# Optimization experiments

Measured on AMD Instinct MI355X. Metric: run time of the kernel, lower is better.

## Reference

```python
import jax, jax.numpy as jnp
import numpy as np

B, D_IN, D_OUT = 8192, 4096, 4096
IN_DIMS = (64, 64)
OUT_DIMS = (64, 64)
# tt_rank_rate=0.5 over dims [64,64,64,64] -> ranks [1,32,1024,32,1]
RANKS = (1, 32, 1024, 32, 1)


def _kaiming_uniform(key, shape):
    # matches nn.init.kaiming_uniform_(a=sqrt(5)) on a (r_prev, d, r) tensor:
    # fan_in = prod(shape[1:]) = d * r, gain = sqrt(2/(1+5)) = sqrt(1/3)
    fan_in = shape[1] * shape[2]
    bound = np.sqrt(1.0 / 3.0) * np.sqrt(3.0 / fan_in)
    return jax.random.uniform(key, shape, jnp.float32, -bound, bound)


def setup_inputs() -> dict:
    key = jax.random.key(0)
    kx, k0, k1, k2, k3, kb = jax.random.split(key, 6)
    dims = list(IN_DIMS) + list(OUT_DIMS)
    shapes = [(RANKS[i], dims[i], RANKS[i + 1]) for i in range(4)]
    x = jax.random.normal(kx, (B, D_IN), jnp.float32)
    core0 = _kaiming_uniform(k0, shapes[0])  # (1, 64, 32)
    core1 = _kaiming_uniform(k1, shapes[1])  # (32, 64, 1024)
    core2 = _kaiming_uniform(k2, shapes[2])  # (1024, 64, 32)
    core3 = _kaiming_uniform(k3, shapes[3])  # (32, 64, 1)
    bb = 1.0 / np.sqrt(D_IN)
    bias = jax.random.uniform(kb, (D_OUT,), jnp.float32, -bb, bb)
    return {"x": x, "core0": core0, "core1": core1, "core2": core2,
            "core3": core3, "bias": bias}


def reference(x, core0, core1, core2, core3, bias):
    b = x.shape[0]
    s = x.reshape(b, IN_DIMS[0], IN_DIMS[1])          # (B, 64, 64)
    # input core 0: contract first input dim (rank-in = 1 squeezed)
    s = jnp.einsum('bcd,cs->bds', s, core0[0])        # (B, 64, 32)
    # input core 1: contract second input dim and rank
    s = jnp.einsum('bcr,rcs->bs', s, core1)           # (B, 1024)
    # output core 2: expand first output dim
    s = jnp.einsum('br,rAs->bAs', s, core2)           # (B, 64, 32)
    # output core 3: expand second output dim (rank-out = 1 squeezed)
    s = jnp.einsum('bAr,rB->bAB', s, core3[..., 0])   # (B, 64, 64)
    return s.reshape(b, -1) + bias                    # (B, 4096)
```

## Files before the change

kernel.cpp:

```cpp
#include <hip/hip_runtime.h>
#include <hip/hip_bf16.h>


typedef _Float16 h4 __attribute__((ext_vector_type(4)));
typedef _Float16 h8 __attribute__((ext_vector_type(8)));
typedef float f32x4 __attribute__((ext_vector_type(4)));

#define BATCH 8192

__device__ __forceinline__ void gld_lds16(const void* g, void* l) {
  __builtin_amdgcn_global_load_lds(
      (__attribute__((address_space(1))) void*)(g),
      (__attribute__((address_space(3))) void*)(l), 16, 0, 0);
}

__global__ __launch_bounds__(256) void transpose_cast2(
    const float* __restrict__ c1, _Float16* __restrict__ W1t,
    const float* __restrict__ c2, _Float16* __restrict__ W2t) {
  __shared__ float t[64][65];
  const int which = blockIdx.z;
  const float* src = which ? c2 : c1;
  _Float16* dst = which ? W2t : W1t;
  const int K = which ? 1024 : 2048, U = which ? 2048 : 1024;
  const int k0 = (which ? blockIdx.y : blockIdx.x) * 64;
  const int u0 = (which ? blockIdx.x : blockIdx.y) * 64;
  const int tx = threadIdx.x & 63, ty = threadIdx.x >> 6;
  for (int i = ty; i < 64; i += 4) {
    const int k = k0 + i;
    const int sr = which ? k : ((k & 31) * 64 + (k >> 5));
    t[i][tx] = src[(size_t)sr * U + u0 + tx];
  }
  __syncthreads();
  for (int i = ty; i < 64; i += 4) {
    dst[(size_t)(u0 + i) * K + k0 + tx] = (_Float16)t[tx][i];
  }
}

__global__ __launch_bounds__(256) void stage2(const float* __restrict__ x,
                                              const float* __restrict__ c0,
                                              _Float16* __restrict__ s1) {
  __shared__ _Float16 xh[4 * 4096];
  __shared__ float c0l[2048];
  const int b0 = blockIdx.x * 4;
  const int tid = threadIdx.x;

  {
    const float4* xg = (const float4*)(x + (size_t)b0 * 4096);
#pragma unroll
    for (int k = 0; k < 16; ++k) {
      float4 v = xg[tid + 256 * k];
      h4 w = {(_Float16)v.x, (_Float16)v.y, (_Float16)v.z, (_Float16)v.w};
      ((h4*)xh)[tid + 256 * k] = w;
    }
    ((float4*)c0l)[tid] = ((const float4*)c0)[tid];
    ((float4*)c0l)[tid + 256] = ((const float4*)c0)[tid + 256];
  }
  __syncthreads();

  const int row = tid >> 6, t6 = tid & 63;
  const int d0 = (t6 >> 3) * 8;
  const int r0 = (t6 & 7) * 4;
  const _Float16* xrow = xh + row * 4096;

  float acc[8][4];
#pragma unroll
  for (int i = 0; i < 8; ++i)
#pragma unroll
    for (int j = 0; j < 4; ++j) acc[i][j] = 0.0f;

  for (int c = 0; c < 64; ++c) {
    h8 xv = *(const h8*)&xrow[c * 64 + d0];
    f32x4 wv = *(const f32x4*)&c0l[c * 32 + r0];
#pragma unroll
    for (int i = 0; i < 8; ++i) {
      const float xf = (float)xv[i];
#pragma unroll
      for (int j = 0; j < 4; ++j) acc[i][j] += xf * wv[j];
    }
  }

  _Float16* s1row = s1 + (size_t)(b0 + row) * 2048;
#pragma unroll
  for (int i = 0; i < 8; ++i) {
    h4 o = {(_Float16)acc[i][0], (_Float16)acc[i][1], (_Float16)acc[i][2],
            (_Float16)acc[i][3]};
    *(h4*)&s1row[(d0 + i) * 32 + r0] = o;
  }
}

template <int M, int N, int K>
__global__ __launch_bounds__(256, 3) void gemm_tn(
    const _Float16* __restrict__ A, const _Float16* __restrict__ Bt,
    _Float16* __restrict__ C) {
  __shared__ _Float16 lA[128 * 64];
  __shared__ _Float16 lB[128 * 64];
  const int bm = blockIdx.x, bn = blockIdx.y;
  const int tid = threadIdx.x;
  const int w = tid >> 6, lane = tid & 63;
  const int wm = (w >> 1) << 6, wn = (w & 1) << 6;
  const int lr = lane & 15, kh = lane >> 4;

  f32x4 acc[4][4] = {};

  const int sr = (w << 5) + (lane >> 3);
  const int sc = ((lane & 7) ^ (lane >> 3)) << 4;
  const char* gA = (const char*)(A + (size_t)(bm * 128 + sr) * K) + sc;
  const char* gB = (const char*)(Bt + (size_t)(bn * 128 + sr) * K) + sc;
  char* lAw = (char*)lA + w * 4096;
  char* lBw = (char*)lB + w * 4096;

  for (int kt = 0; kt < K / 64; ++kt) {
    __syncthreads();
    const size_t go = (size_t)kt * 128;
#pragma unroll
    for (int i = 0; i < 4; ++i) {
      gld_lds16(gA + go + (size_t)(i * 8) * (K * 2), lAw + i * 1024);
      gld_lds16(gB + go + (size_t)(i * 8) * (K * 2), lBw + i * 1024);
    }
    __syncthreads();
#pragma unroll
    for (int kk = 0; kk < 2; ++kk) {
      h8 af[4], bf[4];
#pragma unroll
      for (int m = 0; m < 4; ++m) {
        const int R = wm + m * 16 + lr;
        af[m] = *(const h8*)((const char*)lA + R * 128 +
                             ((((kk << 2) + kh) ^ (R & 7)) << 4));
      }
#pragma unroll
      for (int n = 0; n < 4; ++n) {
        const int R = wn + n * 16 + lr;
        bf[n] = *(const h8*)((const char*)lB + R * 128 +
                             ((((kk << 2) + kh) ^ (R & 7)) << 4));
      }
#pragma unroll
      for (int m = 0; m < 4; ++m)
#pragma unroll
        for (int n = 0; n < 4; ++n)
          acc[m][n] = __builtin_amdgcn_mfma_f32_16x16x32_f16(af[m], bf[n],
                                                             acc[m][n], 0, 0, 0);
    }
  }

#pragma unroll
  for (int m = 0; m < 4; ++m) {
    const int r0 = bm * 128 + wm + m * 16 + kh * 4;
#pragma unroll
    for (int n = 0; n < 4; ++n) {
      const int c0 = bn * 128 + wn + n * 16 + lr;
#pragma unroll
      for (int q = 0; q < 4; ++q)
        C[(size_t)(r0 + q) * N + c0] = (_Float16)acc[m][n][q];
    }
  }
}

template <int M, int K>
__global__ __launch_bounds__(256, 3) void gemm2_fused(
    const _Float16* __restrict__ A, const _Float16* __restrict__ Bt,
    const float* __restrict__ c3, const float* __restrict__ bias,
    float* __restrict__ out) {
  __shared__ _Float16 lds[128 * 128];
  _Float16* lA = lds;
  _Float16* lB = lds + 128 * 64;
  const int bm = blockIdx.x, bn = blockIdx.y;
  const int tid = threadIdx.x;
  const int w = tid >> 6, lane = tid & 63;
  const int wm = (w >> 1) << 6, wn = (w & 1) << 6;
  const int lr = lane & 15, kh = lane >> 4;

  f32x4 acc[4][4] = {};

  const int sr = (w << 5) + (lane >> 3);
  const int sc = ((lane & 7) ^ (lane >> 3)) << 4;
  const char* gA = (const char*)(A + (size_t)(bm * 128 + sr) * K) + sc;
  const char* gB = (const char*)(Bt + (size_t)(bn * 128 + sr) * K) + sc;
  char* lAw = (char*)lA + w * 4096;
  char* lBw = (char*)lB + w * 4096;

  for (int kt = 0; kt < K / 64; ++kt) {
    __syncthreads();
    const size_t go = (size_t)kt * 128;
#pragma unroll
    for (int i = 0; i < 4; ++i) {
      gld_lds16(gA + go + (size_t)(i * 8) * (K * 2), lAw + i * 1024);
      gld_lds16(gB + go + (size_t)(i * 8) * (K * 2), lBw + i * 1024);
    }
    __syncthreads();
#pragma unroll
    for (int kk = 0; kk < 2; ++kk) {
      h8 af[4], bf[4];
#pragma unroll
      for (int m = 0; m < 4; ++m) {
        const int R = wm + m * 16 + lr;
        af[m] = *(const h8*)((const char*)lA + R * 128 +
                             ((((kk << 2) + kh) ^ (R & 7)) << 4));
      }
#pragma unroll
      for (int n = 0; n < 4; ++n) {
        const int R = wn + n * 16 + lr;
        bf[n] = *(const h8*)((const char*)lB + R * 128 +
                             ((((kk << 2) + kh) ^ (R & 7)) << 4));
      }
#pragma unroll
      for (int m = 0; m < 4; ++m)
#pragma unroll
        for (int n = 0; n < 4; ++n)
          acc[m][n] = __builtin_amdgcn_mfma_f32_16x16x32_f16(af[m], bf[n],
                                                             acc[m][n], 0, 0, 0);
    }
  }

  __syncthreads();

  h8 bfe[4];
  float bb[4][4];
#pragma unroll
  for (int n = 0; n < 4; ++n) {
#pragma unroll
    for (int j = 0; j < 8; ++j)
      bfe[n][j] = (_Float16)c3[(kh * 8 + j) * 64 + n * 16 + lr];
#pragma unroll
    for (int a = 0; a < 4; ++a)
      bb[a][n] = bias[bn * 256 + a * 64 + n * 16 + lr];
  }

#pragma unroll
  for (int m = 0; m < 4; ++m) {
    const int Rb = wm + m * 16 + kh * 4;
#pragma unroll
    for (int n = 0; n < 4; ++n) {
      const int cc = wn + n * 16 + lr;
#pragma unroll
      for (int q = 0; q < 4; ++q) {
        const int R = Rb + q;
        const int byte =
            R * 256 + ((((cc >> 3) ^ (R & 7)) << 4) | ((cc & 7) << 1));
        *(_Float16*)((char*)lds + byte) = (_Float16)acc[m][n][q];
      }
    }
  }
  __syncthreads();

  const int wrow = w << 5;
#pragma unroll
  for (int mi = 0; mi < 2; ++mi) {
    const int row = wrow + mi * 16 + lr;
    const int orow0 = bm * 128 + wrow + mi * 16 + kh * 4;
#pragma unroll
    for (int a = 0; a < 4; ++a) {
      h8 af = *(const h8*)((const char*)lds + row * 256 +
                           ((((a << 2) + kh) ^ (row & 7)) << 4));
#pragma unroll
      for (int n = 0; n < 4; ++n) {
        f32x4 d = {};
        d = __builtin_amdgcn_mfma_f32_16x16x32_f16(af, bfe[n], d, 0, 0, 0);
        const int ocol = bn * 256 + a * 64 + n * 16 + lr;
#pragma unroll
        for (int q = 0; q < 4; ++q)
          out[(size_t)(orow0 + q) * 4096 + ocol] = d[q] + bb[a][n];
      }
    }
  }
}

extern "C" void kernel_launch(void* const* d_in, const int* in_sizes, int n_in,
                              void* d_out, int out_size, void* d_ws,
                              size_t ws_size, hipStream_t stream) {
  (void)in_sizes; (void)n_in; (void)out_size; (void)ws_size;
  const float* x     = (const float*)d_in[0];
  const float* core0 = (const float*)d_in[1];
  const float* core1 = (const float*)d_in[2];
  const float* core2 = (const float*)d_in[3];
  const float* core3 = (const float*)d_in[4];
  const float* bias  = (const float*)d_in[5];
  float* out = (float*)d_out;

  char* ws = (char*)d_ws;
  _Float16* s1h = (_Float16*)ws;
  _Float16* s2h = (_Float16*)(ws + 33554432);
  _Float16* W1t = (_Float16*)(ws + 50331648);
  _Float16* W2t = (_Float16*)(ws + 54525952);

  transpose_cast2<<<dim3(32, 16, 2), 256, 0, stream>>>(core1, W1t, core2, W2t);
  stage2<<<BATCH / 4, 256, 0, stream>>>(x, core0, s1h);
  gemm_tn<BATCH, 1024, 2048><<<dim3(BATCH / 128, 1024 / 128), 256, 0, stream>>>(s1h, W1t, s2h);
  gemm2_fused<BATCH, 1024><<<dim3(BATCH / 128, 2048 / 128), 256, 0, stream>>>(s2h, W2t, core3, bias, out);
}
```

Before: 150.0 us.

## Merge GEMMs into triple-buffered 512-thread kernel with 128x256 tiles

Both GEMM kernels become one templated kernel that uses 8 waves per block and 128x256 output tiles. Global-to-LDS loads are triple-buffered so the next tile's loads overlap the current tile's MFMA work, with one barrier per k-step instead of two. It also adds explicit waitcnt, sched_barrier and setprio hints. The 144KB of LDS per block limits occupancy, and fewer blocks in the N dimension lowers the total block count.

Measured after the change: 155.5 us. 1.04x slower.

```diff
diff --git a/kernel.cpp b/kernel.cpp
--- a/kernel.cpp
+++ b/kernel.cpp
@@ -88,174 +88,140 @@
   }
 }
 
-template <int M, int N, int K>
-__global__ __launch_bounds__(256, 3) void gemm_tn(
+template <int K, int CN, bool FUSED>
+__global__ __launch_bounds__(512, 2) void gemm_pipe(
     const _Float16* __restrict__ A, const _Float16* __restrict__ Bt,
-    _Float16* __restrict__ C) {
-  __shared__ _Float16 lA[128 * 64];
-  __shared__ _Float16 lB[128 * 64];
+    _Float16* __restrict__ C, const float* __restrict__ c3,
+    const float* __restrict__ bias, float* __restrict__ out) {
+  __shared__ __align__(16) char lds[3 * 49152];
+  constexpr int NT = K / 64;
   const int bm = blockIdx.x, bn = blockIdx.y;
   const int tid = threadIdx.x;
   const int w = tid >> 6, lane = tid & 63;
-  const int wm = (w >> 1) << 6, wn = (w & 1) << 6;
   const int lr = lane & 15, kh = lane >> 4;
+  const int wmo = (w >> 2) << 6, wno = (w & 3) << 6;
 
   f32x4 acc[4][4] = {};
 
-  const int sr = (w << 5) + (lane >> 3);
-  const int sc = ((lane & 7) ^ (lane >> 3)) << 4;
+  const int sr = tid >> 3;
+  const int sc = ((tid & 7) ^ (sr & 7)) << 4;
   const char* gA = (const char*)(A + (size_t)(bm * 128 + sr) * K) + sc;
-  const char* gB = (const char*)(Bt + (size_t)(bn * 128 + sr) * K) + sc;
-  char* lAw = (char*)lA + w * 4096;
-  char* lBw = (char*)lB + w * 4096;
-
-  for (int kt = 0; kt < K / 64; ++kt) {
+  const char* gB = (const char*)(Bt + (size_t)(bn * 256 + sr) * K) + sc;
+  const size_t rk = (size_t)K * 128;
+  char* lw = lds + (w << 10);
+
+  auto STAGE = [&](int t) {
+    char* b_ = lw + (t % 3) * 49152;
+    const char* ga = gA + (size_t)t * 128;
+    const char* gb = gB + (size_t)t * 128;
+    gld_lds16(ga, b_);
+    gld_lds16(ga + rk, b_ + 8192);
+    gld_lds16(gb, b_ + 16384);
+    gld_lds16(gb + rk, b_ + 24576);
+    gld_lds16(gb + 2 * rk, b_ + 32768);
+    gld_lds16(gb + 3 * rk, b_ + 40960);
+  };
+
+  auto KSTEP = [&](int t) {
+    const char* bufA = lds + (t % 3) * 49152;
+    const char* bufB = bufA + 16384;
+    h8 af[2][4], bf[2][4];
+#pragma unroll
+    for (int kk = 0; kk < 2; ++kk) {
+#pragma unroll
+      for (int m = 0; m < 4; ++m) {
+        const int R = wmo + m * 16 + lr;
+        af[kk][m] = *(const h8*)(bufA + R * 128 +
+                                 ((((kk << 2) + kh) ^ (R & 7)) << 4));
+      }
+#pragma unroll
+      for (int n = 0; n < 4; ++n) {
+        const int R = wno + n * 16 + lr;
+        bf[kk][n] = *(const h8*)(bufB + R * 128 +
+                                 ((((kk << 2) + kh) ^ (R & 7)) << 4));
+      }
+    }
+    asm volatile("s_waitcnt lgkmcnt(0)" ::: "memory");
+    __builtin_amdgcn_sched_barrier(0);
+    __builtin_amdgcn_s_setprio(1);
+#pragma unroll
+    for (int kk = 0; kk < 2; ++kk)
+#pragma unroll
+      for (int m = 0; m < 4; ++m)
+#pragma unroll
+        for (int n = 0; n < 4; ++n)
+          acc[m][n] = __builtin_amdgcn_mfma_f32_16x16x32_f16(
+              af[kk][m], bf[kk][n], acc[m][n], 0, 0, 0);
+    __builtin_amdgcn_s_setprio(0);
+    __builtin_amdgcn_sched_barrier(0);
+  };
+
+  STAGE(0);
+  STAGE(1);
+  for (int t = 0; t < NT - 1; ++t) {
+    asm volatile("s_waitcnt vmcnt(6)" ::: "memory");
+    __builtin_amdgcn_s_barrier();
+    __builtin_amdgcn_sched_barrier(0);
+    if (t < NT - 2) STAGE(t + 2);
+    KSTEP(t);
+  }
+  asm volatile("s_waitcnt vmcnt(0)" ::: "memory");
+  __builtin_amdgcn_s_barrier();
+  __builtin_amdgcn_sched_barrier(0);
+  KSTEP(NT - 1);
+
+  if constexpr (!FUSED) {
+#pragma unroll
+    for (int m = 0; m < 4; ++m) {
+      const int r0 = bm * 128 + wmo + m * 16 + kh * 4;
+#pragma unroll
+      for (int n = 0; n < 4; ++n) {
+        const int c0 = bn * 256 + wno + n * 16 + lr;
+#pragma unroll
+        for (int q = 0; q < 4; ++q)
+          C[(size_t)(r0 + q) * CN + c0] = (_Float16)acc[m][n][q];
+      }
+    }
+  } else {
+    h8 bfe[4];
+    float bb[8][4];
+#pragma unroll
+    for (int n = 0; n < 4; ++n) {
+#pragma unroll
+      for (int j = 0; j < 8; ++j)
+        bfe[n][j] = (_Float16)c3[(kh * 8 + j) * 64 + n * 16 + lr];
+#pragma unroll
+      for (int a = 0; a < 8; ++a)
+        bb[a][n] = bias[(bn * 8 + a) * 64 + n * 16 + lr];
+    }
     __syncthreads();
-    const size_t go = (size_t)kt * 128;
-#pragma unroll
-    for (int i = 0; i < 4; ++i) {
-      gld_lds16(gA + go + (size_t)(i * 8) * (K * 2), lAw + i * 1024);
-      gld_lds16(gB + go + (size_t)(i * 8) * (K * 2), lBw + i * 1024);
+#pragma unroll
+    for (int m = 0; m < 4; ++m) {
+      const int Rb = wmo + m * 16 + kh * 4;
+#pragma unroll
+      for (int n = 0; n < 4; ++n) {
+        const int cc = wno + n * 16 + lr;
+#pragma unroll
+        for (int q = 0; q < 4; ++q) {
+          const int R = Rb + q;
+          *(_Float16*)(lds + R * 512 +
+                       ((((cc >> 3) ^ (R & 7)) << 4) | ((cc & 7) << 1))) =
+              (_Float16)acc[m][n][q];
+        }
+      }
     }
     __syncthreads();
-#pragma unroll
-    for (int kk = 0; kk < 2; ++kk) {
-      h8 af[4], bf[4];
-#pragma unroll
-      for (int m = 0; m < 4; ++m) {
-        const int R = wm + m * 16 + lr;
-        af[m] = *(const h8*)((const char*)lA + R * 128 +
-                             ((((kk << 2) + kh) ^ (R & 7)) << 4));
-      }
-#pragma unroll
-      for (int n = 0; n < 4; ++n) {
-        const int R = wn + n * 16 + lr;
-        bf[n] = *(const h8*)((const char*)lB + R * 128 +
-                             ((((kk << 2) + kh) ^ (R & 7)) << 4));
-      }
-#pragma unroll
-      for (int m = 0; m < 4; ++m)
-#pragma unroll
-        for (int n = 0; n < 4; ++n)
-          acc[m][n] = __builtin_amdgcn_mfma_f32_16x16x32_f16(af[m], bf[n],
-                                                             acc[m][n], 0, 0, 0);
-    }
-  }
-
-#pragma unroll
-  for (int m = 0; m < 4; ++m) {
-    const int r0 = bm * 128 + wm + m * 16 + kh * 4;
-#pragma unroll
-    for (int n = 0; n < 4; ++n) {
-      const int c0 = bn * 128 + wn + n * 16 + lr;
-#pragma unroll
-      for (int q = 0; q < 4; ++q)
-        C[(size_t)(r0 + q) * N + c0] = (_Float16)acc[m][n][q];
-    }
-  }
-}
-
-template <int M, int K>
-__global__ __launch_bounds__(256, 3) void gemm2_fused(
-    const _Float16* __restrict__ A, const _Float16* __restrict__ Bt,
-    const float* __restrict__ c3, const float* __restrict__ bias,
-    float* __restrict__ out) {
-  __shared__ _Float16 lds[128 * 128];
-  _Float16* lA = lds;
-  _Float16* lB = lds + 128 * 64;
-  const int bm = blockIdx.x, bn = blockIdx.y;
-  const int tid = threadIdx.x;
-  const int w = tid >> 6, lane = tid & 63;
-  const int wm = (w >> 1) << 6, wn = (w & 1) << 6;
-  const int lr = lane & 15, kh = lane >> 4;
-
-  f32x4 acc[4][4] = {};
-
-  const int sr = (w << 5) + (lane >> 3);
-  const int sc = ((lane & 7) ^ (lane >> 3)) << 4;
-  const char* gA = (const char*)(A + (size_t)(bm * 128 + sr) * K) + sc;
-  const char* gB = (const char*)(Bt + (size_t)(bn * 128 + sr) * K) + sc;
-  char* lAw = (char*)lA + w * 4096;
-  char* lBw = (char*)lB + w * 4096;
-
-  for (int kt = 0; kt < K / 64; ++kt) {
-    __syncthreads();
-    const size_t go = (size_t)kt * 128;
-#pragma unroll
-    for (int i = 0; i < 4; ++i) {
-      gld_lds16(gA + go + (size_t)(i * 8) * (K * 2), lAw + i * 1024);
-      gld_lds16(gB + go + (size_t)(i * 8) * (K * 2), lBw + i * 1024);
-    }
-    __syncthreads();
-#pragma unroll
-    for (int kk = 0; kk < 2; ++kk) {
-      h8 af[4], bf[4];
-#pragma unroll
-      for (int m = 0; m < 4; ++m) {
-        const int R = wm + m * 16 + lr;
-        af[m] = *(const h8*)((const char*)lA + R * 128 +
-                             ((((kk << 2) + kh) ^ (R & 7)) << 4));
-      }
-#pragma unroll
-      for (int n = 0; n < 4; ++n) {
-        const int R = wn + n * 16 + lr;
-        bf[n] = *(const h8*)((const char*)lB + R * 128 +
-                             ((((kk << 2) + kh) ^ (R & 7)) << 4));
-      }
-#pragma unroll
-      for (int m = 0; m < 4; ++m)
-#pragma unroll
-        for (int n = 0; n < 4; ++n)
-          acc[m][n] = __builtin_amdgcn_mfma_f32_16x16x32_f16(af[m], bf[n],
-                                                             acc[m][n], 0, 0, 0);
-    }
-  }
-
-  __syncthreads();
-
-  h8 bfe[4];
-  float bb[4][4];
-#pragma unroll
-  for (int n = 0; n < 4; ++n) {
-#pragma unroll
-    for (int j = 0; j < 8; ++j)
-      bfe[n][j] = (_Float16)c3[(kh * 8 + j) * 64 + n * 16 + lr];
-#pragma unroll
-    for (int a = 0; a < 4; ++a)
-      bb[a][n] = bias[bn * 256 + a * 64 + n * 16 + lr];
-  }
-
-#pragma unroll
-  for (int m = 0; m < 4; ++m) {
-    const int Rb = wm + m * 16 + kh * 4;
-#pragma unroll
-    for (int n = 0; n < 4; ++n) {
-      const int cc = wn + n * 16 + lr;
-#pragma unroll
-      for (int q = 0; q < 4; ++q) {
-        const int R = Rb + q;
-        const int byte =
-            R * 256 + ((((cc >> 3) ^ (R & 7)) << 4) | ((cc & 7) << 1));
-        *(_Float16*)((char*)lds + byte) = (_Float16)acc[m][n][q];
-      }
-    }
-  }
-  __syncthreads();
-
-  const int wrow = w << 5;
-#pragma unroll
-  for (int mi = 0; mi < 2; ++mi) {
-    const int row = wrow + mi * 16 + lr;
-    const int orow0 = bm * 128 + wrow + mi * 16 + kh * 4;
-#pragma unroll
-    for (int a = 0; a < 4; ++a) {
-      h8 af = *(const h8*)((const char*)lds + row * 256 +
-                           ((((a << 2) + kh) ^ (row & 7)) << 4));
+    const int row = (w << 4) + lr;
+    const int orow0 = bm * 128 + (w << 4) + (kh << 2);
+#pragma unroll
+    for (int a = 0; a < 8; ++a) {
+      h8 afv = *(const h8*)(lds + row * 512 +
+                            ((((a << 2) + kh) ^ (row & 7)) << 4));
 #pragma unroll
       for (int n = 0; n < 4; ++n) {
         f32x4 d = {};
-        d = __builtin_amdgcn_mfma_f32_16x16x32_f16(af, bfe[n], d, 0, 0, 0);
-        const int ocol = bn * 256 + a * 64 + n * 16 + lr;
+        d = __builtin_amdgcn_mfma_f32_16x16x32_f16(afv, bfe[n], d, 0, 0, 0);
+        const int ocol = (bn * 8 + a) * 64 + n * 16 + lr;
 #pragma unroll
         for (int q = 0; q < 4; ++q)
           out[(size_t)(orow0 + q) * 4096 + ocol] = d[q] + bb[a][n];
@@ -284,6 +250,8 @@
 
   transpose_cast2<<<dim3(32, 16, 2), 256, 0, stream>>>(core1, W1t, core2, W2t);
   stage2<<<BATCH / 4, 256, 0, stream>>>(x, core0, s1h);
-  gemm_tn<BATCH, 1024, 2048><<<dim3(BATCH / 128, 1024 / 128), 256, 0, stream>>>(s1h, W1t, s2h);
-  gemm2_fused<BATCH, 1024><<<dim3(BATCH / 128, 2048 / 128), 256, 0, stream>>>(s2h, W2t, core3, bias, out);
-}
+  gemm_pipe<2048, 1024, false><<<dim3(BATCH / 128, 4), 512, 0, stream>>>(
+      s1h, W1t, s2h, nullptr, nullptr, nullptr);
+  gemm_pipe<1024, 4096, true><<<dim3(BATCH / 128, 8), 512, 0, stream>>>(
+      s2h, W2t, nullptr, core3, bias, out);
+}
```
